# Performance work log

Hardware: AMD Instinct MI355X
Metric: run time of the kernel (lower is better)

The kernel has to match this reference:

```python
import jax, jax.numpy as jnp
import numpy as np

R = 0.2          # stable-distribution hash bucket width
TABLE_SIZE = 2   # hash table size (buckets)
M = 5            # number of appended ALSH transform dims
EPS = 1e-12


def conv2d(x, W, b, pad):
    out = jax.lax.conv_general_dilated(
        x, W, window_strides=(1, 1), padding=[(pad, pad), (pad, pad)],
        dimension_numbers=('NCHW', 'OIHW', 'NCHW'))
    return out + b[None, :, None, None]


def maxpool2(x):
    return jax.lax.reduce_window(x, -jnp.inf, jax.lax.max,
                                 (1, 1, 2, 2), (1, 1, 2, 2), 'VALID')


def alsh_mask(x, W, a, c):
    """ALSH filter selection: hash P(kernels) and Q(query) with a stable
    distribution hash h(v)=floor((a.v+b)/r) mod table_size; active filters
    are those landing in the query's bucket. Returns [B, Cout] 0/1 mask.
    Multiplying conv output by this mask == gather active filters then
    zero_fill_missing back to full channel count."""
    Cout, Cin, kH, kW = W.shape
    Kf = W.reshape(Cout, -1)                       # [Cout, Cin*kH*kW]
    norms = jnp.linalg.norm(Kf, axis=1)
    Kn = Kf / (jnp.max(norms) + EPS)               # scale so all norms <= 1
    n = jnp.linalg.norm(Kn, axis=1, keepdims=True)
    # P transform: append norm^2, norm^4, ..., norm^(2^M)
    powers = jnp.concatenate([n ** (2 ** (i + 1)) for i in range(M)], axis=1)
    P = jnp.concatenate([Kn, powers], axis=1)      # [Cout, d+M]
    kh = jnp.mod(jnp.floor((P @ a + c[0]) / R), TABLE_SIZE)  # [Cout]
    # query vector: per-sample channel means broadcast over kernel support
    cm = x.mean(axis=(2, 3))                       # [B, Cin]
    q = jnp.repeat(cm, kH * kW, axis=1)            # [B, Cin*kH*kW] (cin,kh,kw order)
    qn = q / (jnp.linalg.norm(q, axis=1, keepdims=True) + EPS)
    # Q transform: append M halves
    Qv = jnp.concatenate([qn, jnp.full((q.shape[0], M), 0.5, q.dtype)], axis=1)
    qh = jnp.mod(jnp.floor((Qv @ a + c[0]) / R), TABLE_SIZE)  # [B]
    return (kh[None, :] == qh[:, None]).astype(x.dtype)       # [B, Cout]


def setup_inputs() -> dict:
    key = jax.random.key(0)
    ks = jax.random.split(key, 16)
    u = lambda k, s: jax.random.uniform(k, s, jnp.float32, 0.0, R)
    n = lambda k, s, sc=0.1: jax.random.normal(k, s, jnp.float32) * sc
    return {
        'x': jax.random.normal(ks[0], (4096, 3, 32, 32), jnp.float32),
        'W1': n(ks[1], (16, 3, 5, 5)), 'b1': n(ks[2], (16,)),
        'a1': jax.random.normal(ks[3], (80,), jnp.float32), 'c1': u(ks[4], (1,)),
        'W2': n(ks[5], (20, 16, 5, 5)), 'b2': n(ks[6], (20,)),
        'a2': jax.random.normal(ks[7], (405,), jnp.float32), 'c2': u(ks[8], (1,)),
        'W3': n(ks[9], (20, 20, 5, 5)), 'b3': n(ks[10], (20,)),
        'a3': jax.random.normal(ks[11], (505,), jnp.float32), 'c3': u(ks[12], (1,)),
        'Wo': n(ks[13], (10, 320)), 'bo': n(ks[14], (10,)),
    }


def reference(x, W1, b1, a1, c1, W2, b2, a2, c2, W3, b3, a3, c3, Wo, bo):
    m1 = alsh_mask(x, W1, a1, c1)
    h = jax.nn.relu(conv2d(x, W1, b1, 2)) * m1[:, :, None, None]
    h = maxpool2(h)                                # [B,16,16,16]
    m2 = alsh_mask(h, W2, a2, c2)
    h = jax.nn.relu(conv2d(h, W2, b2, 2)) * m2[:, :, None, None]
    h = maxpool2(h)                                # [B,20,8,8]
    m3 = alsh_mask(h, W3, a3, c3)
    h = jax.nn.relu(conv2d(h, W3, b3, 2)) * m3[:, :, None, None]
    # zero_fill_missing -> identity here: inactive channels already zero
    h = maxpool2(h)                                # [B,20,4,4]
    flat = h.reshape(h.shape[0], -1)               # [B,320]
    return flat @ Wo.T + bo
```

## Files before the change

kernel.cpp:

```cpp
#include <hip/hip_runtime.h>
#include <hip/hip_bf16.h>

#define EPSV 1e-12
#define RHASH 0.2

__device__ __forceinline__ int fmod2(double t) {
    return (int)(((long long)floor(t)) & 1LL);
}

__device__ __forceinline__ void load_row6(const float* base, float* r) {
    float2 a0 = *(const float2*)(base);
    float2 a1 = *(const float2*)(base + 2);
    float2 a2 = *(const float2*)(base + 4);
    r[0] = a0.x; r[1] = a0.y; r[2] = a1.x; r[3] = a1.y; r[4] = a2.x; r[5] = a2.y;
}

#define FMA8(c,kx,w) { float wg=(w); \
  acc[c][0]=fmaf(wg,ca[kx],acc[c][0]); acc[c][1]=fmaf(wg,ca[(kx)+1],acc[c][1]); \
  acc[c][2]=fmaf(wg,na[kx],acc[c][2]); acc[c][3]=fmaf(wg,na[(kx)+1],acc[c][3]); \
  acc[c][4]=fmaf(wg,cb[kx],acc[c][4]); acc[c][5]=fmaf(wg,cb[(kx)+1],acc[c][5]); \
  acc[c][6]=fmaf(wg,nb[kx],acc[c][6]); acc[c][7]=fmaf(wg,nb[(kx)+1],acc[c][7]); }

#define FMA4(c,kx,w) { float wg=(w); \
  acc[c][0]=fmaf(wg,cur[kx],acc[c][0]); acc[c][1]=fmaf(wg,cur[(kx)+1],acc[c][1]); \
  acc[c][2]=fmaf(wg,nxt[kx],acc[c][2]); acc[c][3]=fmaf(wg,nxt[(kx)+1],acc[c][3]); }

__device__ void layer_setup(const float* W, const float* a, double cval,
                            int Co, int Ci, int* kh, double* asum, double* qc,
                            double* s_norm, float* Wbuf, float* abuf)
{
    const int t = threadIdx.x;
    const int D = Ci * 25;
    for (int i = t; i < Co * D; i += 256) Wbuf[i] = W[i];
    for (int i = t; i < D + 5; i += 256) abuf[i] = a[i];
    __syncthreads();
    if (t < Co) {
        double s = 0;
        for (int j = 0; j < D; ++j) { double w = (double)Wbuf[t * D + j]; s += w * w; }
        s_norm[t] = sqrt(s);
    }
    __syncthreads();
    if (t == 0) {
        double mx = 0;
        for (int i = 0; i < Co; ++i) mx = fmax(mx, s_norm[i]);
        s_norm[23] = 1.0 / (mx + EPSV);
    }
    __syncthreads();
    double scale = s_norm[23];
    if (t < Co) {
        double dp = 0;
        for (int j = 0; j < D; ++j) dp += (double)Wbuf[t * D + j] * (double)abuf[j];
        dp *= scale;
        double n = s_norm[t] * scale;
        double p = n * n;
        for (int m = 0; m < 5; ++m) { dp += p * (double)abuf[D + m]; p *= p; }
        kh[t] = fmod2((dp + cval) / RHASH);
    }
    if (t >= 64 && t < 64 + Ci) {
        int c = t - 64;
        double s = 0;
        for (int j = 0; j < 25; ++j) s += (double)abuf[c * 25 + j];
        asum[c] = s;
    }
    if (t == 128) {
        double s = 0;
        for (int m = 0; m < 5; ++m) s += (double)abuf[D + m];
        *qc = 0.5 * s + cval;
    }
    __syncthreads();
}

__global__ __launch_bounds__(256) void setup_kernel(
    const float* W1, const float* a1, const float* c1,
    const float* W2, const float* a2, const float* c2,
    const float* W3, const float* a3, const float* c3,
    double* dmeta, int* imeta)
{
    __shared__ float Wbuf[10000];
    __shared__ float abuf[512];
    __shared__ double s_norm[24];
    layer_setup(W1, a1, (double)c1[0], 16, 3,  imeta + 0,  dmeta + 0,  dmeta + 39, s_norm, Wbuf, abuf);
    layer_setup(W2, a2, (double)c2[0], 20, 16, imeta + 16, dmeta + 3,  dmeta + 40, s_norm, Wbuf, abuf);
    layer_setup(W3, a3, (double)c3[0], 20, 20, imeta + 36, dmeta + 19, dmeta + 41, s_norm, Wbuf, abuf);
}

__global__ __launch_bounds__(256) void pack_kernel(const float* W1, const float* W2, const float* W3,
                                                   float* Wp1, float* Wp2, float* Wp3)
{
    int i = blockIdx.x * 256 + threadIdx.x;
    if (i < 1200) {
        int co = i & 15, r = i >> 4;
        int kx = r % 5, r2 = r / 5, ky = r2 % 5, ci = r2 / 5;
        Wp1[i] = W1[co * 75 + ci * 25 + ky * 5 + kx];
    } else if (i < 1200 + 8960) {
        int k = i - 1200;
        int j = k % 28, r = k / 28;
        int cog = r % 4, r2 = r / 4, ky = r2 % 5, ci = r2 / 5;
        Wp2[k] = (j < 25) ? W2[(cog * 5 + j / 5) * 400 + ci * 25 + ky * 5 + (j % 5)] : 0.f;
    } else if (i < 1200 + 8960 + 11200) {
        int k = i - 10160;
        int j = k % 28, r = k / 28;
        int cog = r % 4, r2 = r / 4, ky = r2 % 5, ci = r2 / 5;
        Wp3[k] = (j < 25) ? W3[(cog * 5 + j / 5) * 500 + ci * 25 + ky * 5 + (j % 5)] : 0.f;
    }
}

__global__ __launch_bounds__(256) void conv1_kernel(
    const float* __restrict__ x, const float* __restrict__ Wp1,
    const float* __restrict__ b1, const int* __restrict__ kh1,
    const double* __restrict__ dmeta, float* __restrict__ h1,
    int* __restrict__ qh2)
{
    __shared__ float xs[3][36][36];
    __shared__ float Ws[1200];
    __shared__ double s_red[3];
    __shared__ double s_ch[16][4];

    const int b = blockIdx.x, t = threadIdx.x;
    const int w = t >> 6, ln = t & 63;

    for (int i = t; i < 3 * 36 * 36; i += 256) (&xs[0][0][0])[i] = 0.f;
    for (int i = t; i < 600; i += 256) ((float2*)Ws)[i] = ((const float2*)Wp1)[i];
    __syncthreads();
    const float2* xb2 = (const float2*)(x + (size_t)b * 3072);
    for (int i = t; i < 1536; i += 256) {
        int idx = i * 2, c = idx >> 10, rem = idx & 1023;
        *(float2*)&xs[c][(rem >> 5) + 2][(rem & 31) + 2] = xb2[i];
    }
    __syncthreads();

    if (w < 3) {
        double s = 0;
        for (int j = 0; j < 16; ++j) {
            int i = ln + 64 * j;
            s += (double)xs[w][(i >> 5) + 2][(i & 31) + 2];
        }
        #pragma unroll
        for (int off = 32; off; off >>= 1) s += __shfl_xor(s, off);
        if (ln == 0) s_red[w] = s;
    }
    __syncthreads();
    double dp = 0, nn = 0;
    #pragma unroll
    for (int c = 0; c < 3; ++c) {
        double cm = s_red[c] * (1.0 / 1024.0);
        dp += cm * dmeta[c]; nn += cm * cm;
    }
    const int qh = fmod2((dp / (5.0 * sqrt(nn) + EPSV) + dmeta[39]) / RHASH);

    const int cog = ln >> 5;
    const int py = 4 * w + ((ln >> 3) & 3), pxp = ln & 7;
    const int y0 = 2 * py, x0a = 2 * pxp, x0b = 2 * pxp + 16;

    float acc[8][8];
    #pragma unroll
    for (int c = 0; c < 8; ++c) {
        float bb = b1[cog * 8 + c];
        #pragma unroll
        for (int j = 0; j < 8; ++j) acc[c][j] = bb;
    }

    #pragma unroll
    for (int ci = 0; ci < 3; ++ci) {
        #pragma unroll
        for (int ky = 0; ky < 5; ++ky) {
            float ca[6], na[6], cb[6], nb[6];
            load_row6(&xs[ci][y0 + ky][x0a],     ca);
            load_row6(&xs[ci][y0 + ky + 1][x0a], na);
            load_row6(&xs[ci][y0 + ky][x0b],     cb);
            load_row6(&xs[ci][y0 + ky + 1][x0b], nb);
            const float4* wq = (const float4*)&Ws[((ci * 5 + ky) * 5) * 16 + cog * 8];
            #pragma unroll
            for (int kx = 0; kx < 5; ++kx) {
                float4 w0 = wq[kx * 4];
                float4 w1 = wq[kx * 4 + 1];
                FMA8(0, kx, w0.x) FMA8(1, kx, w0.y) FMA8(2, kx, w0.z) FMA8(3, kx, w0.w)
                FMA8(4, kx, w1.x) FMA8(5, kx, w1.y) FMA8(6, kx, w1.z) FMA8(7, kx, w1.w)
            }
        }
    }

    float* hb = h1 + (size_t)b * 4096 + py * 16 + pxp;
    double csum[8];
    #pragma unroll
    for (int c = 0; c < 8; ++c) {
        int co = cog * 8 + c;
        float mask = (kh1[co] == qh) ? 1.f : 0.f;
        float mA = fmaxf(fmaxf(acc[c][0], acc[c][1]), fmaxf(acc[c][2], acc[c][3]));
        float mB = fmaxf(fmaxf(acc[c][4], acc[c][5]), fmaxf(acc[c][6], acc[c][7]));
        float vA = fmaxf(mA, 0.f) * mask;
        float vB = fmaxf(mB, 0.f) * mask;
        hb[co * 256]     = vA;
        hb[co * 256 + 8] = vB;
        csum[c] = (double)vA + (double)vB;
    }
    #pragma unroll
    for (int c = 0; c < 8; ++c) {
        double s = csum[c];
        #pragma unroll
        for (int off = 16; off; off >>= 1) s += __shfl_xor(s, off);
        if ((ln & 31) == 0) s_ch[cog * 8 + c][w] = s;
    }
    __syncthreads();
    if (t == 0) {
        double dp2 = 0, nn2 = 0;
        #pragma unroll
        for (int c = 0; c < 16; ++c) {
            double cm = (s_ch[c][0] + s_ch[c][1] + s_ch[c][2] + s_ch[c][3]) * (1.0 / 256.0);
            dp2 += cm * dmeta[3 + c]; nn2 += cm * cm;
        }
        qh2[b] = fmod2((dp2 / (5.0 * sqrt(nn2) + EPSV) + dmeta[40]) / RHASH);
    }
}

__global__ __launch_bounds__(256) void conv2_kernel(
    const float* __restrict__ h1, const float* __restrict__ Wp2,
    const float* __restrict__ b2, const int* __restrict__ kh2,
    const int* __restrict__ qh2, const double* __restrict__ dmeta,
    float* __restrict__ h2, int* __restrict__ qh3)
{
    __shared__ float xs[8][20][20];
    __shared__ float Ws[4480];
    __shared__ double s_ch[20][4];

    const int b = blockIdx.x, t = threadIdx.x;
    const int w = t >> 6, l = t & 63;
    const int cog = l >> 4;
    const int pos = w * 16 + (l & 15);
    const int py = pos >> 3, px = pos & 7;
    const int y0 = 2 * py, x0 = 2 * px;

    for (int i = t; i < 3200; i += 256) (&xs[0][0][0])[i] = 0.f;

    const int qh = qh2[b];
    float acc[5][4];
    #pragma unroll
    for (int c = 0; c < 5; ++c) {
        float bb = b2[cog * 5 + c];
        acc[c][0] = bb; acc[c][1] = bb; acc[c][2] = bb; acc[c][3] = bb;
    }
    __syncthreads();

    for (int ch = 0; ch < 2; ++ch) {
        for (int i = t; i < 2240; i += 256)
            ((float2*)Ws)[i] = ((const float2*)(Wp2 + ch * 4480))[i];
        const float2* src = (const float2*)(h1 + (size_t)b * 4096 + ch * 2048);
        for (int i = t; i < 1024; i += 256) {
            int ci = i >> 7, r = i & 127, p2 = r * 2;
            *(float2*)&xs[ci][(p2 >> 4) + 2][(p2 & 15) + 2] = src[i];
        }
        __syncthreads();

        for (int ci = 0; ci < 8; ++ci) {
            #pragma unroll
            for (int ky = 0; ky < 5; ++ky) {
                float xr0[6], xr1[6];
                load_row6(&xs[ci][y0 + ky][x0],     xr0);
                load_row6(&xs[ci][y0 + ky + 1][x0], xr1);
                float wv[28];
                const float4* wp = (const float4*)&Ws[((ci * 5 + ky) * 4 + cog) * 28];
                *(float4*)&wv[0]  = wp[0];
                *(float4*)&wv[4]  = wp[1];
                *(float4*)&wv[8]  = wp[2];
                *(float4*)&wv[12] = wp[3];
                *(float4*)&wv[16] = wp[4];
                *(float4*)&wv[20] = wp[5];
                *(float4*)&wv[24] = wp[6];
                #pragma unroll
                for (int c = 0; c < 5; ++c) {
                    #pragma unroll
                    for (int kx = 0; kx < 5; ++kx) {
                        float wgt = wv[c * 5 + kx];
                        acc[c][0] = fmaf(wgt, xr0[kx],     acc[c][0]);
                        acc[c][1] = fmaf(wgt, xr0[kx + 1], acc[c][1]);
                        acc[c][2] = fmaf(wgt, xr1[kx],     acc[c][2]);
                        acc[c][3] = fmaf(wgt, xr1[kx + 1], acc[c][3]);
                    }
                }
            }
        }
        __syncthreads();
    }

    float* ob = h2 + (size_t)b * 1280 + pos;
    double csum[5];
    #pragma unroll
    for (int c = 0; c < 5; ++c) {
        int co = cog * 5 + c;
        float mask = (kh2[co] == qh) ? 1.f : 0.f;
        float m = fmaxf(fmaxf(acc[c][0], acc[c][1]), fmaxf(acc[c][2], acc[c][3]));
        float v = fmaxf(m, 0.f) * mask;
        ob[co * 64] = v;
        csum[c] = (double)v;
    }
    #pragma unroll
    for (int c = 0; c < 5; ++c) {
        double sv = csum[c];
        #pragma unroll
        for (int off = 8; off; off >>= 1) sv += __shfl_xor(sv, off);
        if ((l & 15) == 0) s_ch[cog * 5 + c][w] = sv;
    }
    __syncthreads();
    if (t == 0) {
        double dp2 = 0, nn2 = 0;
        #pragma unroll
        for (int c = 0; c < 20; ++c) {
            double cm = (s_ch[c][0] + s_ch[c][1] + s_ch[c][2] + s_ch[c][3]) * (1.0 / 64.0);
            dp2 += cm * dmeta[19 + c]; nn2 += cm * cm;
        }
        qh3[b] = fmod2((dp2 / (5.0 * sqrt(nn2) + EPSV) + dmeta[41]) / RHASH);
    }
}

__global__ __launch_bounds__(256) void conv3_kernel(
    const float* __restrict__ h2, const float* __restrict__ Wp3,
    const float* __restrict__ b3, const int* __restrict__ kh3,
    const int* __restrict__ qh3,
    const float* __restrict__ Wo, const float* __restrict__ bo,
    float* __restrict__ out, int B)
{
    __shared__ float xs[4][5][12][12];
    __shared__ float Ws[2800];
    __shared__ float flat[4][320];

    const int b0 = blockIdx.x * 4, t = threadIdx.x;
    const int s = t >> 6, q0 = t & 63, cog = q0 >> 4, pos = q0 & 15;
    const int py = pos >> 2, px = pos & 3;
    const int y0 = 2 * py, x0 = 2 * px;
    const int b = b0 + s;

    for (int i = t; i < 4 * 5 * 144; i += 256) (&xs[0][0][0][0])[i] = 0.f;

    const int qh = (b < B) ? qh3[b] : 0;
    float acc[5][4];
    #pragma unroll
    for (int c = 0; c < 5; ++c) {
        float bb = b3[cog * 5 + c];
        acc[c][0] = bb; acc[c][1] = bb; acc[c][2] = bb; acc[c][3] = bb;
    }
    __syncthreads();

    for (int ch = 0; ch < 4; ++ch) {
        for (int i = t; i < 1400; i += 256)
            ((float2*)Ws)[i] = ((const float2*)(Wp3 + ch * 2800))[i];
        for (int i = t; i < 640; i += 256) {
            int ss = i / 160, r = i - ss * 160, ci = r >> 5, rr = r & 31, p2 = rr * 2;
            if (b0 + ss < B)
                *(float2*)&xs[ss][ci][(p2 >> 3) + 2][(p2 & 7) + 2] =
                    ((const float2*)(h2 + (size_t)(b0 + ss) * 1280 + (ch * 5 + ci) * 64))[rr];
        }
        __syncthreads();

        #pragma unroll
        for (int ci = 0; ci < 5; ++ci) {
            float cur[6], nxt[6];
            load_row6(&xs[s][ci][y0][x0], cur);
            load_row6(&xs[s][ci][y0 + 1][x0], nxt);
            #pragma unroll
            for (int ky = 0; ky < 5; ++ky) {
                const float* wrow = &Ws[((ci * 5 + ky) * 4 + cog) * 28];
                const float4* wq = (const float4*)wrow;
                float4 q;
                q = wq[0]; FMA4(0, 0, q.x) FMA4(0, 1, q.y) FMA4(0, 2, q.z) FMA4(0, 3, q.w)
                q = wq[1]; FMA4(0, 4, q.x) FMA4(1, 0, q.y) FMA4(1, 1, q.z) FMA4(1, 2, q.w)
                q = wq[2]; FMA4(1, 3, q.x) FMA4(1, 4, q.y) FMA4(2, 0, q.z) FMA4(2, 1, q.w)
                q = wq[3]; FMA4(2, 2, q.x) FMA4(2, 3, q.y) FMA4(2, 4, q.z) FMA4(3, 0, q.w)
                q = wq[4]; FMA4(3, 1, q.x) FMA4(3, 2, q.y) FMA4(3, 3, q.z) FMA4(3, 4, q.w)
                q = wq[5]; FMA4(4, 0, q.x) FMA4(4, 1, q.y) FMA4(4, 2, q.z) FMA4(4, 3, q.w)
                FMA4(4, 4, wrow[24])
                if (ky < 4) {
                    #pragma unroll
                    for (int j = 0; j < 6; ++j) cur[j] = nxt[j];
                    load_row6(&xs[s][ci][y0 + ky + 2][x0], nxt);
                }
            }
        }
        __syncthreads();
    }

    #pragma unroll
    for (int c = 0; c < 5; ++c) {
        int co = cog * 5 + c;
        float m = fmaxf(fmaxf(acc[c][0], acc[c][1]), fmaxf(acc[c][2], acc[c][3]));
        flat[s][co * 16 + pos] = fmaxf(m, 0.f) * ((kh3[co] == qh) ? 1.f : 0.f);
    }
    __syncthreads();

    if (t < 160) {
        const int g = t >> 2, qq = t & 3;
        const int ss = g / 10, o = g - ss * 10;
        float a = 0.f;
        const float* wr = Wo + o * 320;
        for (int k = qq; k < 320; k += 4) a = fmaf(flat[ss][k], wr[k], a);
        a += __shfl_xor(a, 1);
        a += __shfl_xor(a, 2);
        if (qq == 0 && b0 + ss < B) out[(size_t)(b0 + ss) * 10 + o] = a + bo[o];
    }
}

extern "C" void kernel_launch(void* const* d_in, const int* in_sizes, int n_in,
                              void* d_out, int out_size, void* d_ws, size_t ws_size,
                              hipStream_t stream)
{
    const float* x  = (const float*)d_in[0];
    const float* W1 = (const float*)d_in[1];
    const float* b1 = (const float*)d_in[2];
    const float* a1 = (const float*)d_in[3];
    const float* c1 = (const float*)d_in[4];
    const float* W2 = (const float*)d_in[5];
    const float* b2 = (const float*)d_in[6];
    const float* a2 = (const float*)d_in[7];
    const float* c2 = (const float*)d_in[8];
    const float* W3 = (const float*)d_in[9];
    const float* b3 = (const float*)d_in[10];
    const float* a3 = (const float*)d_in[11];
    const float* c3 = (const float*)d_in[12];
    const float* Wo = (const float*)d_in[13];
    const float* bo = (const float*)d_in[14];
    float* out = (float*)d_out;

    const int B = in_sizes[0] / 3072;

    float* h1  = (float*)d_ws;
    float* h2  = h1 + (size_t)B * 4096;
    float* Wp1 = h2 + (size_t)B * 1280;
    float* Wp2 = Wp1 + 1200;
    float* Wp3 = Wp2 + 8960;
    double* dmeta = (double*)(Wp3 + 11200);
    int* imeta = (int*)(dmeta + 42);
    int* qh2 = imeta + 56;
    int* qh3 = qh2 + B;

    setup_kernel<<<1, 256, 0, stream>>>(W1, a1, c1, W2, a2, c2, W3, a3, c3, dmeta, imeta);
    pack_kernel<<<84, 256, 0, stream>>>(W1, W2, W3, Wp1, Wp2, Wp3);
    conv1_kernel<<<B, 256, 0, stream>>>(x, Wp1, b1, imeta, dmeta, h1, qh2);
    conv2_kernel<<<B, 256, 0, stream>>>(h1, Wp2, b2, imeta + 16, qh2, dmeta, h2, qh3);
    conv3_kernel<<<(B + 3) / 4, 256, 0, stream>>>(h2, Wp3, b3, imeta + 36, qh3, Wo, bo, out, B);
}
```

Baseline: 539.1 us.

## Batch four samples per block in conv2 and widen per-thread output tile

conv2 now has each block process four samples, one per wavefront, and each thread computes a strip of 4 pooled outputs (8x2 conv outputs) for 5 channels. Input rows are held in registers and slid down across ky, so fewer shared loads are needed per FMA. Each weight tile loaded into shared memory is also reused across four samples, and outputs are written as float4. The cost is 80 accumulators per thread, which raises register pressure and may lower occupancy, and there are four times fewer blocks.

```diff
diff --git a/kernel.cpp b/kernel.cpp
--- a/kernel.cpp
+++ b/kernel.cpp
@@ -13,6 +13,11 @@
     float2 a1 = *(const float2*)(base + 2);
     float2 a2 = *(const float2*)(base + 4);
     r[0] = a0.x; r[1] = a0.y; r[2] = a1.x; r[3] = a1.y; r[4] = a2.x; r[5] = a2.y;
+}
+
+__device__ __forceinline__ void load_row12(const float* base, float* r) {
+    #pragma unroll
+    for (int j = 0; j < 6; ++j) *(float2*)&r[2 * j] = *(const float2*)(base + 2 * j);
 }
 
 #define FMA8(c,kx,w) { float wg=(w); \
@@ -217,48 +222,50 @@
     const float* __restrict__ h1, const float* __restrict__ Wp2,
     const float* __restrict__ b2, const int* __restrict__ kh2,
     const int* __restrict__ qh2, const double* __restrict__ dmeta,
-    float* __restrict__ h2, int* __restrict__ qh3)
-{
-    __shared__ float xs[8][20][20];
-    __shared__ float Ws[4480];
-    __shared__ double s_ch[20][4];
-
-    const int b = blockIdx.x, t = threadIdx.x;
-    const int w = t >> 6, l = t & 63;
-    const int cog = l >> 4;
-    const int pos = w * 16 + (l & 15);
-    const int py = pos >> 3, px = pos & 7;
-    const int y0 = 2 * py, x0 = 2 * px;
-
-    for (int i = t; i < 3200; i += 256) (&xs[0][0][0])[i] = 0.f;
-
-    const int qh = qh2[b];
-    float acc[5][4];
+    float* __restrict__ h2, int* __restrict__ qh3, int B)
+{
+    __shared__ float xs[4][4][20][22];
+    __shared__ float Ws[2240];
+    __shared__ double s_ch[4][20];
+
+    const int b0 = blockIdx.x * 4, t = threadIdx.x;
+    const int s = t >> 6, l = t & 63;
+    const int cog = l >> 4, pos = l & 15;
+    const int py = pos >> 1, pxg = pos & 1;
+    const int b = b0 + s;
+
+    for (int i = t; i < 4 * 4 * 20 * 22; i += 256) (&xs[0][0][0][0])[i] = 0.f;
+
+    const int qh = (b < B) ? qh2[b] : 0;
+    float accA[5][8], accB[5][8];
     #pragma unroll
     for (int c = 0; c < 5; ++c) {
         float bb = b2[cog * 5 + c];
-        acc[c][0] = bb; acc[c][1] = bb; acc[c][2] = bb; acc[c][3] = bb;
-    }
-    __syncthreads();
-
-    for (int ch = 0; ch < 2; ++ch) {
-        for (int i = t; i < 2240; i += 256)
-            ((float2*)Ws)[i] = ((const float2*)(Wp2 + ch * 4480))[i];
-        const float2* src = (const float2*)(h1 + (size_t)b * 4096 + ch * 2048);
-        for (int i = t; i < 1024; i += 256) {
-            int ci = i >> 7, r = i & 127, p2 = r * 2;
-            *(float2*)&xs[ci][(p2 >> 4) + 2][(p2 & 15) + 2] = src[i];
+        #pragma unroll
+        for (int k = 0; k < 8; ++k) { accA[c][k] = bb; accB[c][k] = bb; }
+    }
+    __syncthreads();
+
+    for (int ch = 0; ch < 4; ++ch) {
+        for (int i = t; i < 1120; i += 256)
+            ((float2*)Ws)[i] = ((const float2*)(Wp2 + ch * 2240))[i];
+        for (int i = t; i < 2048; i += 256) {
+            int si = i >> 9, rem = i & 511, cil = rem >> 7, rr = rem & 127;
+            int p2 = rr * 2, row = p2 >> 4, col = p2 & 15;
+            if (b0 + si < B)
+                *(float2*)&xs[si][cil][row + 2][col + 2] =
+                    ((const float2*)(h1 + (size_t)(b0 + si) * 4096 + (size_t)(ch * 4 + cil) * 256))[rr];
         }
         __syncthreads();
 
-        for (int ci = 0; ci < 8; ++ci) {
+        for (int cil = 0; cil < 4; ++cil) {
+            float ra[12], rb[12];
+            load_row12(&xs[s][cil][2 * py][8 * pxg],     ra);
+            load_row12(&xs[s][cil][2 * py + 1][8 * pxg], rb);
             #pragma unroll
             for (int ky = 0; ky < 5; ++ky) {
-                float xr0[6], xr1[6];
-                load_row6(&xs[ci][y0 + ky][x0],     xr0);
-                load_row6(&xs[ci][y0 + ky + 1][x0], xr1);
                 float wv[28];
-                const float4* wp = (const float4*)&Ws[((ci * 5 + ky) * 4 + cog) * 28];
+                const float4* wp = (const float4*)&Ws[((cil * 5 + ky) * 4 + cog) * 28];
                 *(float4*)&wv[0]  = wp[0];
                 *(float4*)&wv[4]  = wp[1];
                 *(float4*)&wv[8]  = wp[2];
@@ -270,42 +277,52 @@
                 for (int c = 0; c < 5; ++c) {
                     #pragma unroll
                     for (int kx = 0; kx < 5; ++kx) {
-                        float wgt = wv[c * 5 + kx];
-                        acc[c][0] = fmaf(wgt, xr0[kx],     acc[c][0]);
-                        acc[c][1] = fmaf(wgt, xr0[kx + 1], acc[c][1]);
-                        acc[c][2] = fmaf(wgt, xr1[kx],     acc[c][2]);
-                        acc[c][3] = fmaf(wgt, xr1[kx + 1], acc[c][3]);
+                        float wg = wv[c * 5 + kx];
+                        #pragma unroll
+                        for (int k = 0; k < 8; ++k) {
+                            accA[c][k] = fmaf(wg, ra[k + kx], accA[c][k]);
+                            accB[c][k] = fmaf(wg, rb[k + kx], accB[c][k]);
+                        }
                     }
                 }
+                if (ky < 4) {
+                    #pragma unroll
+                    for (int j = 0; j < 12; ++j) ra[j] = rb[j];
+                    load_row12(&xs[s][cil][2 * py + ky + 2][8 * pxg], rb);
+                }
             }
         }
         __syncthreads();
     }
 
-    float* ob = h2 + (size_t)b * 1280 + pos;
+    float* ob = h2 + (size_t)b * 1280 + py * 8 + pxg * 4;
     double csum[5];
     #pragma unroll
     for (int c = 0; c < 5; ++c) {
         int co = cog * 5 + c;
         float mask = (kh2[co] == qh) ? 1.f : 0.f;
-        float m = fmaxf(fmaxf(acc[c][0], acc[c][1]), fmaxf(acc[c][2], acc[c][3]));
-        float v = fmaxf(m, 0.f) * mask;
-        ob[co * 64] = v;
-        csum[c] = (double)v;
+        float v0 = fmaxf(fmaxf(accA[c][0], accA[c][1]), fmaxf(accB[c][0], accB[c][1]));
+        float v1 = fmaxf(fmaxf(accA[c][2], accA[c][3]), fmaxf(accB[c][2], accB[c][3]));
+        float v2 = fmaxf(fmaxf(accA[c][4], accA[c][5]), fmaxf(accB[c][4], accB[c][5]));
+        float v3 = fmaxf(fmaxf(accA[c][6], accA[c][7]), fmaxf(accB[c][6], accB[c][7]));
+        v0 = fmaxf(v0, 0.f) * mask; v1 = fmaxf(v1, 0.f) * mask;
+        v2 = fmaxf(v2, 0.f) * mask; v3 = fmaxf(v3, 0.f) * mask;
+        if (b < B) *(float4*)(ob + co * 64) = make_float4(v0, v1, v2, v3);
+        csum[c] = (double)v0 + (double)v1 + (double)v2 + (double)v3;
     }
     #pragma unroll
     for (int c = 0; c < 5; ++c) {
         double sv = csum[c];
-        #pragma unroll
-        for (int off = 8; off; off >>= 1) sv += __shfl_xor(sv, off);
-        if ((l & 15) == 0) s_ch[cog * 5 + c][w] = sv;
-    }
-    __syncthreads();
-    if (t == 0) {
+        sv += __shfl_xor(sv, 8); sv += __shfl_xor(sv, 4);
+        sv += __shfl_xor(sv, 2); sv += __shfl_xor(sv, 1);
+        if (pos == 0) s_ch[s][cog * 5 + c] = sv;
+    }
+    __syncthreads();
+    if (l == 0 && b < B) {
         double dp2 = 0, nn2 = 0;
         #pragma unroll
         for (int c = 0; c < 20; ++c) {
-            double cm = (s_ch[c][0] + s_ch[c][1] + s_ch[c][2] + s_ch[c][3]) * (1.0 / 64.0);
+            double cm = s_ch[s][c] * (1.0 / 64.0);
             dp2 += cm * dmeta[19 + c]; nn2 += cm * cm;
         }
         qh3[b] = fmod2((dp2 / (5.0 * sqrt(nn2) + EPSV) + dmeta[41]) / RHASH);
@@ -434,6 +451,6 @@
     setup_kernel<<<1, 256, 0, stream>>>(W1, a1, c1, W2, a2, c2, W3, a3, c3, dmeta, imeta);
     pack_kernel<<<84, 256, 0, stream>>>(W1, W2, W3, Wp1, Wp2, Wp3);
     conv1_kernel<<<B, 256, 0, stream>>>(x, Wp1, b1, imeta, dmeta, h1, qh2);
-    conv2_kernel<<<B, 256, 0, stream>>>(h1, Wp2, b2, imeta + 16, qh2, dmeta, h2, qh3);
+    conv2_kernel<<<(B + 3) / 4, 256, 0, stream>>>(h1, Wp2, b2, imeta + 16, qh2, dmeta, h2, qh3, B);
     conv3_kernel<<<(B + 3) / 4, 256, 0, stream>>>(h2, Wp3, b3, imeta + 36, qh3, Wo, bo, out, B);
 }
```

Result: faster. 523.1 us (-3.0%).
